# Performance work log

Hardware: AMD Instinct MI355X
Metric: run time of the kernel (lower is better)

Reference implementation:

```python
import jax, jax.numpy as jnp
import numpy as np

B, L, D, K = 32, 128, 400, 40
RTOL, ATOL = 1e-4, 1e-6


def setup_inputs() -> dict:
    key = jax.random.key(0)
    ks = jax.random.split(key, 9)
    s = 0.3                      # input scale keeps exp(energy) in fp32 range
    u = 1.0 / np.sqrt(D)         # param scale
    input_h = jax.random.normal(ks[0], (B, L, D), jnp.float32) * s
    input_c = jax.random.normal(ks[1], (B, L, D), jnp.float32) * s
    W_d = jax.random.normal(ks[2], (K, D), jnp.float32) * u
    W_e = jax.random.normal(ks[3], (K, D), jnp.float32) * u
    U = jax.random.normal(ks[4], (K, D, D), jnp.float32) * u
    b = jax.random.normal(ks[5], (K,), jnp.float32) * 0.1
    heads = jax.random.randint(ks[6], (B, L), 0, L)
    pos = jnp.arange(L)[None, :]
    heads = jnp.where(heads == pos, (heads + 1) % L, heads)  # no self-loops (diag is -inf)
    arc_tags = jax.random.randint(ks[7], (B, L), 0, K)
    lengths = jax.random.randint(ks[8], (B,), L // 2, L + 1)
    mask = (jnp.arange(L)[None, :] < lengths[:, None]).astype(jnp.float32)
    return {"input_h": input_h, "input_c": input_c, "W_d": W_d, "W_e": W_e,
            "U": U, "b": b, "mask": mask, "heads": heads,
            "arc_tags": arc_tags, "lengths": lengths}


def reference(input_h, input_c, W_d, W_e, U, b, mask, heads, arc_tags, lengths):
    Bsz, Ln, _ = input_h.shape
    # --- BiAAttention: energy[b,k,head,child] ---
    bil = jnp.einsum('bhd,kde,bce->bkhc', input_h, U, input_c)
    sd = jnp.einsum('kd,bhd->bkh', W_d, input_h)[:, :, :, None]   # head bias
    se = jnp.einsum('kd,bcd->bkc', W_e, input_c)[:, :, None, :]   # child bias
    energy = bil + sd + se + b[None, :, None, None]
    energy = energy * mask[:, None, :, None] * mask[:, None, None, :]
    eye = jnp.eye(Ln, dtype=energy.dtype)
    energy = energy + jnp.where(eye > 0, -jnp.inf, 0.0)           # no self-arcs
    # --- Matrix-Tree partition function ---
    A = jnp.exp(energy) * mask[:, None, :, None] * mask[:, None, None, :]
    A = A.sum(axis=1)                                             # [B,L,L] over labels
    Dg = A.sum(axis=1) * (1.0 + RTOL) + ATOL                      # column (in-degree) sums
    Lap = eye * Dg[:, None, :] - A                                # Laplacian
    Sub = Lap[:, 1:, 1:]                                          # drop root row/col
    valid = jnp.arange(Ln - 1)[None, :] < (lengths - 1)[:, None]
    vm = valid[:, :, None] & valid[:, None, :]
    Sub = jnp.where(vm, Sub, jnp.eye(Ln - 1, dtype=Sub.dtype))    # identity-pad = logdet of [1:len,1:len]
    z = jnp.linalg.slogdet(Sub)[1]                                # [B]
    # --- gold-tree energy ---
    bi = jnp.arange(Bsz)[:, None]
    pos = jnp.arange(Ln)[None, :]
    te = energy[bi, arc_tags, heads, pos]                         # [B,L]
    tgt = te[:, 1:].sum(axis=1)
    return z - tgt
```

## Files before the change

kernel.cpp:

```cpp
#include <hip/hip_runtime.h>
#include <hip/hip_bf16.h>

#define BB 32
#define LL 128
#define DD 400
#define KK 40
#define EE 416
#define SDN 50
#define SEN 52

typedef __attribute__((ext_vector_type(8)))  short  bfrag;
typedef __attribute__((ext_vector_type(16))) float  ffrag;

static __device__ __forceinline__ short f2bf(float f) {
    union { float f; unsigned u; } v; v.f = f;
    unsigned r = (v.u + 0x7FFF + ((v.u >> 16) & 1)) >> 16;
    return (short)r;
}

#define MFMA32(a, b, c) __builtin_amdgcn_mfma_f32_32x32x16_bf16((a), (b), (c), 0, 0, 0)

static __device__ __forceinline__ void fzero(ffrag& f) {
#pragma unroll
    for (int r = 0; r < 16; ++r) f[r] = 0.f;
}

__global__ __launch_bounds__(256) void p_prep(
    const float* __restrict__ H, const float* __restrict__ C,
    const float* __restrict__ U,
    short* __restrict__ Hs, short* __restrict__ Cs, short* __restrict__ Us)
{
    int id = blockIdx.x * 256 + threadIdx.x;
    if (id < BB*SDN*LL) {
        int b = id / (SDN*LL); int r = id % (SDN*LL);
        int sd = r / LL; int h = r % LL;
        const float* src = H + ((size_t)(b*LL + h))*DD + sd*8;
        bfrag v;
#pragma unroll
        for (int j = 0; j < 8; ++j) v[j] = f2bf(src[j]);
        *(bfrag*)(Hs + (size_t)id*8) = v;
    } else if (id < BB*SDN*LL + BB*SEN*LL) {
        id -= BB*SDN*LL;
        int b = id / (SEN*LL); int r = id % (SEN*LL);
        int se = r / LL; int c = r % LL;
        bfrag v;
#pragma unroll
        for (int j = 0; j < 8; ++j) {
            int e = se*8 + j;
            v[j] = (e < DD) ? f2bf(C[((size_t)(b*LL + c))*DD + e]) : (short)0;
        }
        *(bfrag*)(Cs + (size_t)id*8) = v;
    } else {
        id -= BB*SDN*LL + BB*SEN*LL;
        int k = id / (SDN*EE); int r = id % (SDN*EE);
        int sd = r / EE; int e = r % EE;
        bfrag v;
#pragma unroll
        for (int j = 0; j < 8; ++j)
            v[j] = (e < DD) ? f2bf(U[((size_t)k*DD + sd*8 + j)*DD + e]) : (short)0;
        *(bfrag*)(Us + (size_t)id*8) = v;
    }
}

__global__ __launch_bounds__(256) void k_sdse(
    const float* __restrict__ H, const float* __restrict__ C,
    const float* __restrict__ Wd, const float* __restrict__ We,
    float* __restrict__ SD, float* __restrict__ SE)
{
    const int b   = blockIdx.x;
    const int rg  = blockIdx.y;
    const int srcC = blockIdx.z;
    const int t = threadIdx.x;

    __shared__ float Wl[KK*DD];
    {
        const float4* Wsrc = (const float4*)(srcC ? We : Wd);
        for (int i = t; i < KK*DD/4; i += 256) ((float4*)Wl)[i] = Wsrc[i];
    }
    __syncthreads();

    const int task = t >> 3;
    const int p    = t & 7;
    const int row  = rg*32 + task;
    const float* X = (srcC ? C : H) + ((size_t)(b*LL + row))*DD + p*50;

    float2 x[25];
#pragma unroll
    for (int i = 0; i < 25; ++i) x[i] = ((const float2*)X)[i];

    float* out = (srcC ? SE : SD) + (size_t)b*KK*LL + row;
    const float* Wb = Wl + p*50;

    for (int k = 0; k < KK; ++k) {
        const float2* wp = (const float2*)(Wb + k*DD);
        float s0 = 0.f, s1 = 0.f;
#pragma unroll
        for (int i = 0; i < 24; i += 2) {
            float2 w0 = wp[i], w1 = wp[i+1];
            s0 = fmaf(x[i].x,   w0.x, s0); s0 = fmaf(x[i].y,   w0.y, s0);
            s1 = fmaf(x[i+1].x, w1.x, s1); s1 = fmaf(x[i+1].y, w1.y, s1);
        }
        { float2 w0 = wp[24]; s0 = fmaf(x[24].x, w0.x, s0); s0 = fmaf(x[24].y, w0.y, s0); }
        float s = s0 + s1;
        s += __shfl_xor(s, 1); s += __shfl_xor(s, 2); s += __shfl_xor(s, 4);
        if (p == 0) out[k*LL] = s;
    }
}

static __device__ __forceinline__ void t_write(
    short* __restrict__ Ping, const ffrag& T, int et, int ht, int l31, int kh)
{
#pragma unroll
    for (int r = 0; r < 16; r += 2) {
        const int e_loc = 32*et + (r&3) + 8*(r>>2) + 4*kh;
        if (e_loc < DD) {
            unsigned lo = (unsigned short)f2bf(T[r]);
            unsigned hi = (unsigned short)f2bf(T[r+1]);
            *(unsigned*)(&Ping[((size_t)(e_loc>>3)*LL + 32*ht + l31)*8 + (e_loc&7)]) =
                lo | (hi << 16);
        }
    }
}

__global__ __launch_bounds__(1024) void k_mfma(
    const short* __restrict__ Hs, const short* __restrict__ Cs,
    const short* __restrict__ Us,
    const float* __restrict__ SD, const float* __restrict__ SE,
    const float* __restrict__ bvec, const float* __restrict__ mask,
    const int* __restrict__ heads, const int* __restrict__ tags,
    float* __restrict__ A8, float* __restrict__ tgt)
{
    const int b  = blockIdx.x;
    const int g  = blockIdx.y;
    const int t  = threadIdx.x;
    const int w  = t >> 6;
    const int l31 = t & 31;
    const int kh  = (t >> 5) & 1;

    __shared__ short Ping[SDN*LL*8];

    const size_t hsB = (size_t)b * SDN * LL;
    const size_t csB = (size_t)b * SEN * LL;

    const int ht2 = w >> 2;
    const int ct  = w & 3;
    const int hbase = 32*ht2 + 4*kh;
    const int c0 = 32*ct + l31;
    const float mc0 = mask[b*LL + c0];
    const int head0 = heads[b*LL + c0];
    const int tag0  = tags[b*LL + c0];
    unsigned vb = 0;
#pragma unroll
    for (int r = 0; r < 16; ++r) {
        const int hr = hbase + (r&3) + 8*(r>>2);
        if (mask[b*LL + hr] != 0.f && mc0 != 0.f && hr != c0) vb |= 1u << r;
    }

    ffrag E; fzero(E);

    for (int kk = 0; kk < 5; ++kk) {
        const int k = g + 8*kk;

        __syncthreads();

        {
            const uint4* src = (const uint4*)(Hs + hsB*8);
            uint4* dst = (uint4*)Ping;
            for (int i = t; i < SDN*LL*8*2/16; i += 1024) dst[i] = src[i];
        }
        __syncthreads();

        ffrag T0, T1, T2, T3;
        if (w < 13) {
            fzero(T0); fzero(T1); fzero(T2); fzero(T3);
            const int et = w;
            const short* up = Us + (((size_t)k*SDN + kh)*EE + 32*et + l31)*8;
            const short* hb = Ping + ((size_t)kh*LL + l31)*8;
#define UPF(j)    (*(const bfrag*)(up + (size_t)(j)*(2*EE*8)))
#define HPF(j,ht) (*(const bfrag*)(hb + ((size_t)(2*(j))*LL + 32*(ht))*8))
            bfrag a0 = UPF(0), a1 = UPF(1);
#pragma unroll 1
            for (int j = 0; j < 23; ++j) {
                bfrag an = UPF(j+2);
                bfrag b0 = HPF(j,0), b1 = HPF(j,1), b2 = HPF(j,2), b3 = HPF(j,3);
                T0 = MFMA32(a0, b0, T0); T1 = MFMA32(a0, b1, T1);
                T2 = MFMA32(a0, b2, T2); T3 = MFMA32(a0, b3, T3);
                a0 = a1; a1 = an;
            }
            {
                bfrag b0 = HPF(23,0), b1 = HPF(23,1), b2 = HPF(23,2), b3 = HPF(23,3);
                T0 = MFMA32(a0, b0, T0); T1 = MFMA32(a0, b1, T1);
                T2 = MFMA32(a0, b2, T2); T3 = MFMA32(a0, b3, T3);
                b0 = HPF(24,0); b1 = HPF(24,1); b2 = HPF(24,2); b3 = HPF(24,3);
                T0 = MFMA32(a1, b0, T0); T1 = MFMA32(a1, b1, T1);
                T2 = MFMA32(a1, b2, T2); T3 = MFMA32(a1, b3, T3);
            }
#undef UPF
#undef HPF
        }
        __syncthreads();

        if (w < 13) {
            t_write(Ping, T0, w, 0, l31, kh);
            t_write(Ping, T1, w, 1, l31, kh);
            t_write(Ping, T2, w, 2, l31, kh);
            t_write(Ping, T3, w, 3, l31, kh);
        }
        __syncthreads();

        ffrag S; fzero(S);
        const short* ta = Ping + ((size_t)kh*LL + 32*ht2 + l31)*8;
        const short* cp = Cs + (csB + (size_t)kh*LL + 32*ct + l31)*8;
#define TAF(j) (*(const bfrag*)(ta + (size_t)(2*(j))*(LL*8)))
#define CPF(j) (*(const bfrag*)(cp + (size_t)(2*(j))*(LL*8)))
        bfrag c0f = CPF(0), c1f = CPF(1), c2f = CPF(2);
        bfrag t0f = TAF(0), t1f = TAF(1);
#pragma unroll 1
        for (int j = 0; j < 22; ++j) {
            bfrag cn = CPF(j+3);
            bfrag tn = TAF(j+2);
            S = MFMA32(t0f, c0f, S);
            t0f = t1f; t1f = tn;
            c0f = c1f; c1f = c2f; c2f = cn;
        }
        S = MFMA32(t0f, c0f, S);
        S = MFMA32(t1f, c1f, S);
        S = MFMA32(TAF(24), c2f, S);
#undef TAF
#undef CPF

        const float bk = bvec[k];
        const float* SDb = SD + ((size_t)b*KK + k)*LL;
        const float sev = SE[((size_t)b*KK + k)*LL + c0];
#pragma unroll
        for (int r = 0; r < 16; ++r) {
            const int hr = hbase + (r&3) + 8*(r>>2);
            const float ev = S[r] + SDb[hr] + sev + bk;
            if ((vb >> r) & 1) {
                E[r] += __expf(ev);
                if (c0 >= 1 && tag0 == k && head0 == hr) atomicAdd(&tgt[b], ev);
            }
        }
    }

    float* Ab = A8 + ((size_t)(g*BB + b))*LL*LL;
#pragma unroll
    for (int r = 0; r < 16; ++r) {
        const int hr = hbase + (r&3) + 8*(r>>2);
        Ab[hr*LL + c0] = E[r];
    }
}

__global__ __launch_bounds__(256) void k_logdet(
    const float* __restrict__ A8, const int* __restrict__ lengths,
    const float* __restrict__ tgt, float* __restrict__ out)
{
    const int b = blockIdx.x;
    const int t = threadIdx.x;
    const int rg = t >> 4;
    const int cg = t & 15;

    __shared__ float As[LL*LL];
    __shared__ float Dg[128];
    __shared__ float Lbuf[128];
    __shared__ float Ubuf[128];
    __shared__ float red[256];

    const float4* A4 = (const float4*)A8;
    for (int f4 = t; f4 < 4096; f4 += 256) {
        float4 s = make_float4(0.f, 0.f, 0.f, 0.f);
#pragma unroll
        for (int g = 0; g < 8; ++g) {
            float4 v = A4[((size_t)(g*BB + b))*4096 + f4];
            s.x += v.x; s.y += v.y; s.z += v.z; s.w += v.w;
        }
        ((float4*)As)[f4] = s;
    }
    __syncthreads();

    if (t < 128) {
        float s = 0.f;
        for (int hr = 0; hr < LL; ++hr) s += As[hr*LL + t];
        Dg[t] = s * (1.0f + 1e-4f) + 1e-6f;
    }
    __syncthreads();

    const int n1 = lengths[b] - 1;
    float m[8][8];
#pragma unroll
    for (int r = 0; r < 8; ++r) {
        const int i = 8*rg + r;
#pragma unroll
        for (int c = 0; c < 8; ++c) {
            const int j = 8*cg + c;
            float v;
            if (i < n1 && j < n1)
                v = ((i == j) ? Dg[i+1] : 0.f) - As[(i+1)*LL + (j+1)];
            else
                v = (i == j) ? 1.f : 0.f;
            m[r][c] = v;
        }
    }
    __syncthreads();

    for (int j = 0; j < 127; ++j) {
        const int jg = j >> 3, jl = j & 7;
        if (cg == jg) {
#pragma unroll
            for (int c = 0; c < 8; ++c) {
                if (c == jl) {
#pragma unroll
                    for (int r = 0; r < 8; ++r) Lbuf[8*rg + r] = m[r][c];
                }
            }
        }
        if (rg == jg) {
#pragma unroll
            for (int r = 0; r < 8; ++r) {
                if (r == jl) {
#pragma unroll
                    for (int c = 0; c < 8; ++c) Ubuf[8*cg + c] = m[r][c];
                }
            }
        }
        __syncthreads();

        const float piv = Lbuf[j];
        if (t == j) Dg[j] = piv;
        const float rp = 1.0f / piv;
        float lr[8], ur[8];
#pragma unroll
        for (int r = 0; r < 8; ++r) lr[r] = Lbuf[8*rg + r] * rp;
#pragma unroll
        for (int c = 0; c < 8; ++c) ur[c] = Ubuf[8*cg + c];
#pragma unroll
        for (int r = 0; r < 8; ++r)
#pragma unroll
            for (int c = 0; c < 8; ++c)
                m[r][c] = fmaf(-lr[r], ur[c], m[r][c]);
        __syncthreads();
    }

    float lsum = 0.f;
    if (t < 127) lsum = logf(Dg[t]);
    red[t] = lsum;
    __syncthreads();
    for (int off = 128; off >= 1; off >>= 1) {
        if (t < off) red[t] += red[t + off];
        __syncthreads();
    }
    if (t == 0) out[b] = red[0] - tgt[b];
}

extern "C" void kernel_launch(void* const* d_in, const int* in_sizes, int n_in,
                              void* d_out, int out_size, void* d_ws, size_t ws_size,
                              hipStream_t stream) {
    const float* H    = (const float*)d_in[0];
    const float* C    = (const float*)d_in[1];
    const float* Wd   = (const float*)d_in[2];
    const float* We   = (const float*)d_in[3];
    const float* U    = (const float*)d_in[4];
    const float* bv   = (const float*)d_in[5];
    const float* mask = (const float*)d_in[6];
    const int* heads  = (const int*)d_in[7];
    const int* tags   = (const int*)d_in[8];
    const int* lens   = (const int*)d_in[9];
    float* out = (float*)d_out;

    char* p = (char*)d_ws;
    float* A8  = (float*)p;                 p += (size_t)8*BB*LL*LL*4;
    float* tgt = (float*)p;                 p += 32*4;
    float* SDp = (float*)p;                 p += (size_t)BB*KK*LL*4;
    float* SEp = (float*)p;                 p += (size_t)BB*KK*LL*4;
    short* Hsp = (short*)p;                 p += (size_t)BB*SDN*LL*8*2;
    short* Csp = (short*)p;                 p += (size_t)BB*SEN*LL*8*2;
    short* Usp = (short*)p;                 p += (size_t)KK*SDN*EE*8*2;

    hipMemsetAsync(tgt, 0, 32*4, stream);

    p_prep<<<dim3(4882), 256, 0, stream>>>(H, C, U, Hsp, Csp, Usp);
    k_sdse<<<dim3(BB, 4, 2), 256, 0, stream>>>(H, C, Wd, We, SDp, SEp);
    k_mfma<<<dim3(BB, 8), 1024, 0, stream>>>(Hsp, Csp, Usp, SDp, SEp, bv, mask,
                                             heads, tags, A8, tgt);
    k_logdet<<<dim3(BB), 256, 0, stream>>>(A8, lens, tgt, out);
}
```

Measured before the change: 344.9 us.

## Split k_mfma head dimension across two blocks of 512 threads

The bilinear MFMA kernel now launches a third grid dimension that splits the 128 head rows into two halves, each handled by a 512-thread block with half the shared memory. The first-stage U·H work is redistributed as 26 tiles over 8 waves (3-4 tiles each) instead of 13 waves doing four tiles while 3 waves idle. This is meant to raise occupancy and balance work across waves. The cost is that U weights and C fragments are now read twice per batch/label group.

```diff
diff --git a/kernel.cpp b/kernel.cpp
--- a/kernel.cpp
+++ b/kernel.cpp
@@ -107,8 +107,8 @@
     }
 }
 
-static __device__ __forceinline__ void t_write(
-    short* __restrict__ Ping, const ffrag& T, int et, int ht, int l31, int kh)
+static __device__ __forceinline__ void t_write64(
+    short* __restrict__ Ping, const ffrag& T, int et, int th, int l31, int kh)
 {
 #pragma unroll
     for (int r = 0; r < 16; r += 2) {
@@ -116,13 +116,13 @@
         if (e_loc < DD) {
             unsigned lo = (unsigned short)f2bf(T[r]);
             unsigned hi = (unsigned short)f2bf(T[r+1]);
-            *(unsigned*)(&Ping[((size_t)(e_loc>>3)*LL + 32*ht + l31)*8 + (e_loc&7)]) =
+            *(unsigned*)(&Ping[((size_t)(e_loc>>3)*64 + 32*th + l31)*8 + (e_loc&7)]) =
                 lo | (hi << 16);
         }
     }
 }
 
-__global__ __launch_bounds__(1024) void k_mfma(
+__global__ __launch_bounds__(512, 4) void k_mfma(
     const short* __restrict__ Hs, const short* __restrict__ Cs,
     const short* __restrict__ Us,
     const float* __restrict__ SD, const float* __restrict__ SE,
@@ -132,19 +132,20 @@
 {
     const int b  = blockIdx.x;
     const int g  = blockIdx.y;
+    const int hh = blockIdx.z;
     const int t  = threadIdx.x;
     const int w  = t >> 6;
     const int l31 = t & 31;
     const int kh  = (t >> 5) & 1;
 
-    __shared__ short Ping[SDN*LL*8];
+    __shared__ short Ping[SDN*64*8];
 
     const size_t hsB = (size_t)b * SDN * LL;
     const size_t csB = (size_t)b * SEN * LL;
 
     const int ht2 = w >> 2;
     const int ct  = w & 3;
-    const int hbase = 32*ht2 + 4*kh;
+    const int hbase = 64*hh + 32*ht2 + 4*kh;
     const int c0 = 32*ct + l31;
     const float mc0 = mask[b*LL + c0];
     const int head0 = heads[b*LL + c0];
@@ -157,61 +158,60 @@
     }
 
     ffrag E; fzero(E);
+    const int ntiles = (w < 2) ? 4 : 3;
 
     for (int kk = 0; kk < 5; ++kk) {
         const int k = g + 8*kk;
 
         __syncthreads();
 
-        {
-            const uint4* src = (const uint4*)(Hs + hsB*8);
-            uint4* dst = (uint4*)Ping;
-            for (int i = t; i < SDN*LL*8*2/16; i += 1024) dst[i] = src[i];
-        }
-        __syncthreads();
-
-        ffrag T0, T1, T2, T3;
-        if (w < 13) {
-            fzero(T0); fzero(T1); fzero(T2); fzero(T3);
-            const int et = w;
-            const short* up = Us + (((size_t)k*SDN + kh)*EE + 32*et + l31)*8;
-            const short* hb = Ping + ((size_t)kh*LL + l31)*8;
-#define UPF(j)    (*(const bfrag*)(up + (size_t)(j)*(2*EE*8)))
-#define HPF(j,ht) (*(const bfrag*)(hb + ((size_t)(2*(j))*LL + 32*(ht))*8))
-            bfrag a0 = UPF(0), a1 = UPF(1);
+        for (int i = t; i < SDN*64; i += 512) {
+            const int sd = i >> 6, hl = i & 63;
+            *(uint4*)(Ping + (size_t)i*8) =
+                *(const uint4*)(Hs + (hsB + (size_t)sd*LL + 64*hh + hl)*8);
+        }
+        __syncthreads();
+
+        ffrag Ts[4];
+#pragma unroll
+        for (int ti = 0; ti < 4; ++ti) {
+            if (ti < ntiles) {
+                const int tau = w + 8*ti;
+                const int te = tau >> 1;
+                const int th = tau & 1;
+                fzero(Ts[ti]);
+                const short* up = Us + (((size_t)k*SDN + kh)*EE + 32*te + l31)*8;
+                const short* hb = Ping + ((size_t)kh*64 + 32*th + l31)*8;
+#define UPF(j) (*(const bfrag*)(up + (size_t)(j)*(2*EE*8)))
+#define HPF(j) (*(const bfrag*)(hb + (size_t)(2*(j))*(64*8)))
+                bfrag a0 = UPF(0), a1 = UPF(1);
 #pragma unroll 1
-            for (int j = 0; j < 23; ++j) {
-                bfrag an = UPF(j+2);
-                bfrag b0 = HPF(j,0), b1 = HPF(j,1), b2 = HPF(j,2), b3 = HPF(j,3);
-                T0 = MFMA32(a0, b0, T0); T1 = MFMA32(a0, b1, T1);
-                T2 = MFMA32(a0, b2, T2); T3 = MFMA32(a0, b3, T3);
-                a0 = a1; a1 = an;
-            }
-            {
-                bfrag b0 = HPF(23,0), b1 = HPF(23,1), b2 = HPF(23,2), b3 = HPF(23,3);
-                T0 = MFMA32(a0, b0, T0); T1 = MFMA32(a0, b1, T1);
-                T2 = MFMA32(a0, b2, T2); T3 = MFMA32(a0, b3, T3);
-                b0 = HPF(24,0); b1 = HPF(24,1); b2 = HPF(24,2); b3 = HPF(24,3);
-                T0 = MFMA32(a1, b0, T0); T1 = MFMA32(a1, b1, T1);
-                T2 = MFMA32(a1, b2, T2); T3 = MFMA32(a1, b3, T3);
-            }
+                for (int j = 0; j < 23; ++j) {
+                    bfrag an = UPF(j+2);
+                    Ts[ti] = MFMA32(a0, HPF(j), Ts[ti]);
+                    a0 = a1; a1 = an;
+                }
+                Ts[ti] = MFMA32(a0, HPF(23), Ts[ti]);
+                Ts[ti] = MFMA32(a1, HPF(24), Ts[ti]);
 #undef UPF
 #undef HPF
-        }
-        __syncthreads();
-
-        if (w < 13) {
-            t_write(Ping, T0, w, 0, l31, kh);
-            t_write(Ping, T1, w, 1, l31, kh);
-            t_write(Ping, T2, w, 2, l31, kh);
-            t_write(Ping, T3, w, 3, l31, kh);
+            }
+        }
+        __syncthreads();
+
+#pragma unroll
+        for (int ti = 0; ti < 4; ++ti) {
+            if (ti < ntiles) {
+                const int tau = w + 8*ti;
+                t_write64(Ping, Ts[ti], tau >> 1, tau & 1, l31, kh);
+            }
         }
         __syncthreads();
 
         ffrag S; fzero(S);
-        const short* ta = Ping + ((size_t)kh*LL + 32*ht2 + l31)*8;
+        const short* ta = Ping + ((size_t)kh*64 + 32*ht2 + l31)*8;
         const short* cp = Cs + (csB + (size_t)kh*LL + 32*ct + l31)*8;
-#define TAF(j) (*(const bfrag*)(ta + (size_t)(2*(j))*(LL*8)))
+#define TAF(j) (*(const bfrag*)(ta + (size_t)(2*(j))*(64*8)))
 #define CPF(j) (*(const bfrag*)(cp + (size_t)(2*(j))*(LL*8)))
         bfrag c0f = CPF(0), c1f = CPF(1), c2f = CPF(2);
         bfrag t0f = TAF(0), t1f = TAF(1);
@@ -380,7 +380,7 @@
 
     p_prep<<<dim3(4882), 256, 0, stream>>>(H, C, U, Hsp, Csp, Usp);
     k_sdse<<<dim3(BB, 4, 2), 256, 0, stream>>>(H, C, Wd, We, SDp, SEp);
-    k_mfma<<<dim3(BB, 8), 1024, 0, stream>>>(Hsp, Csp, Usp, SDp, SEp, bv, mask,
-                                             heads, tags, A8, tgt);
+    k_mfma<<<dim3(BB, 8, 2), 512, 0, stream>>>(Hsp, Csp, Usp, SDp, SEp, bv, mask,
+                                               heads, tags, A8, tgt);
     k_logdet<<<dim3(BB), 256, 0, stream>>>(A8, lens, tgt, out);
 }
```

Result: slower. 488.2 us (+41.5%).
